# Performance work log

Measured on AMD Instinct MI355X. Metric: run time of the kernel, lower is better.

Reference implementation:

```python
import jax, jax.numpy as jnp
import numpy as np

NUM_EXPERTS = 8
TOP_K = 2
CAPACITY_FACTOR = 1.25
D_MODEL = 2048
HIDDEN = 2048
N_TOKENS = 4096


def _expert_capacity(n_tokens):
    ideal = TOP_K * n_tokens / NUM_EXPERTS
    allowed = int(CAPACITY_FACTOR * ideal)
    return ((allowed + 7) // 8) * 8  # ensure_multiple_of(..., 8)


def setup_inputs() -> dict:
    key = jax.random.key(0)
    ks = jax.random.split(key, 6)
    x = jax.random.normal(ks[0], (N_TOKENS, D_MODEL), dtype=jnp.float32)
    ew = jax.random.uniform(ks[1], (N_TOKENS, TOP_K), dtype=jnp.float32)
    expert_weights = ew / jnp.sum(ew, axis=-1, keepdims=True)  # router softmax-like weights
    expert_indices = jax.random.randint(ks[2], (N_TOKENS, TOP_K), 0, NUM_EXPERTS, dtype=jnp.int32)
    s = 1.0 / np.sqrt(D_MODEL)
    w1 = jax.random.normal(ks[3], (NUM_EXPERTS, D_MODEL, HIDDEN), dtype=jnp.float32) * s
    w3 = jax.random.normal(ks[4], (NUM_EXPERTS, D_MODEL, HIDDEN), dtype=jnp.float32) * s
    w2 = jax.random.normal(ks[5], (NUM_EXPERTS, HIDDEN, D_MODEL), dtype=jnp.float32) * (1.0 / np.sqrt(HIDDEN))
    return {"x": x, "expert_weights": expert_weights, "expert_indices": expert_indices,
            "w1": w1, "w2": w2, "w3": w3}


def reference(x, expert_weights, expert_indices, w1, w2, w3):
    N, d = x.shape
    E = NUM_EXPERTS
    cap = _expert_capacity(N)
    T = N * TOP_K

    flat_e = expert_indices.reshape(-1)                      # [T]
    # histc: tokens per expert
    counts = jnp.zeros((E,), jnp.int32).at[flat_e].add(1)
    # stable sort by expert id (torch.sort on ints is stable here semantically)
    order = jnp.argsort(flat_e, stable=True)                 # [T]
    sorted_e = flat_e[order]
    starts = jnp.cumsum(counts) - counts                     # bin start offsets
    pos = jnp.arange(T, dtype=jnp.int32) - starts[sorted_e]  # rank within expert bin
    valid = pos < cap                                        # drop tokens over capacity
    tok = order // TOP_K                                     # source token per routed slot

    # binned_gather -> [E, cap, d]
    dest = jnp.where(valid, sorted_e * cap + pos, 0)
    xg = jnp.zeros((E * cap, d), x.dtype).at[dest].add(
        jnp.where(valid[:, None], x[tok], 0.0))
    xg = xg.reshape(E, cap, d)

    # grouped SwiGLU MLP per expert
    h = jax.nn.silu(jnp.einsum('ecd,edh->ech', xg, w1)) * jnp.einsum('ecd,edh->ech', xg, w3)
    ye = jnp.einsum('ech,ehd->ecd', h, w2).reshape(E * cap, d)

    # binned_scatter with expert weights (combine)
    w_flat = expert_weights.reshape(-1)[order]               # [T]
    contrib = ye[dest] * (w_flat * valid.astype(x.dtype))[:, None]
    y = jnp.zeros((N, d), x.dtype).at[tok].add(contrib)
    return y, counts
```

## Files before the change

### kernel.cpp

```cpp
#include <hip/hip_runtime.h>
#include <cstdint>

#define NEXP 8
#define TOPK 2
#define NTOK 4096
#define NSLOT (NTOK * TOPK)
#define CAP 1280
#define DM 2048
#define EC (NEXP * CAP)

typedef __bf16 bf16x8 __attribute__((ext_vector_type(8)));
typedef float  f32x4  __attribute__((ext_vector_type(4)));
typedef int    i32x4  __attribute__((ext_vector_type(4)));
typedef int    i32x8  __attribute__((ext_vector_type(8)));

typedef const void __attribute__((address_space(1))) gvoid;
typedef void __attribute__((address_space(3))) lvoid;

__device__ __forceinline__ void gld16(const void* g, void* l) {
  __builtin_amdgcn_global_load_lds((gvoid*)(uintptr_t)g, (lvoid*)(uintptr_t)l,
                                   16, 0, 0);
}

__device__ __forceinline__ unsigned fp8x4(float a, float b, float c, float d) {
  int v = __builtin_amdgcn_cvt_pk_fp8_f32(a, b, 0, false);
  v = __builtin_amdgcn_cvt_pk_fp8_f32(c, d, v, true);
  return (unsigned)v;
}
__device__ __forceinline__ unsigned char fp8one(float a) {
  return (unsigned char)(__builtin_amdgcn_cvt_pk_fp8_f32(a, a, 0, false) & 0xff);
}

__global__ void route_k(const int* __restrict__ eidx, int* __restrict__ row_token,
                        int* __restrict__ slot_dest, int* __restrict__ mcount,
                        float* __restrict__ out) {
  __shared__ int lh[256][NEXP];
  int tid = threadIdx.x;
  for (int i = tid; i < EC; i += 256) row_token[i] = -1;
#pragma unroll
  for (int e = 0; e < NEXP; ++e) lh[tid][e] = 0;
  __syncthreads();
  int base = tid * 32;
  for (int j = 0; j < 32; ++j) lh[tid][eidx[base + j]]++;
  __syncthreads();
  if (tid < NEXP) {
    int run = 0;
    for (int i = 0; i < 256; ++i) { int t = lh[i][tid]; lh[i][tid] = run; run += t; }
    mcount[tid] = run < CAP ? run : CAP;
    out[(size_t)NTOK * DM + tid] = (float)run;
  }
  __syncthreads();
  for (int j = 0; j < 32; ++j) {
    int t = base + j;
    int e = eidx[t];
    int r = lh[tid][e]++;
    if (r < CAP) { int dst = e * CAP + r; slot_dest[t] = dst; row_token[dst] = t >> 1; }
    else slot_dest[t] = -1;
  }
}

__global__ void gather_k(const float* __restrict__ x, const int* __restrict__ row_token,
                         unsigned char* __restrict__ xg) {
  int r = blockIdx.x;
  int c = threadIdx.x * 8;
  int tok = row_token[r];
  uint2 o;
  if (tok >= 0) {
    const float* src = x + (size_t)tok * DM + c;
    float4 a = *(const float4*)src;
    float4 b = *(const float4*)(src + 4);
    o.x = fp8x4(a.x, a.y, a.z, a.w);
    o.y = fp8x4(b.x, b.y, b.z, b.w);
  } else {
    o.x = 0u; o.y = 0u;
  }
  *(uint2*)(xg + (size_t)r * DM + c) = o;
}

__global__ void transT_k(const float* __restrict__ w, unsigned char* __restrict__ wT) {
  __shared__ float t[64][69];
  int e = blockIdx.z;
  int n0 = blockIdx.x * 64, k0 = blockIdx.y * 64;
  const float* src = w + ((size_t)e << 22) + (size_t)k0 * DM + n0;
  unsigned char* dst = wT + ((size_t)e << 22) + (size_t)n0 * DM + k0;
  int c4 = (threadIdx.x & 15) * 4, r0 = threadIdx.x >> 4;
#pragma unroll
  for (int p = 0; p < 4; ++p) {
    int r = p * 16 + r0;
    float4 v = *(const float4*)(src + (size_t)r * DM + c4);
    t[r][c4 + 0] = v.x; t[r][c4 + 1] = v.y; t[r][c4 + 2] = v.z; t[r][c4 + 3] = v.w;
  }
  __syncthreads();
  int j = threadIdx.x & 7, rr0 = threadIdx.x >> 3;
#pragma unroll
  for (int q = 0; q < 2; ++q) {
    int rr = q * 32 + rr0;
    int k8 = j * 8;
    uint2 v;
    v.x = fp8x4(t[k8 + 0][rr], t[k8 + 1][rr], t[k8 + 2][rr], t[k8 + 3][rr]);
    v.y = fp8x4(t[k8 + 4][rr], t[k8 + 5][rr], t[k8 + 6][rr], t[k8 + 7][rr]);
    *(uint2*)(dst + (size_t)rr * DM + k8) = v;
  }
}

template<bool SWI>
__global__ __launch_bounds__(256, 4)
void gemm_k(const unsigned char* __restrict__ A0, const unsigned char* __restrict__ BT,
            void* C, const __bf16* __restrict__ U, const int* __restrict__ mcount) {
  int lbid = blockIdx.x + 16 * (blockIdx.y + 10 * blockIdx.z);
  int nb = (lbid & 7) * 160 + (lbid >> 3);
  int e = nb / 160, rem = nb % 160, mt = rem >> 4, nt = rem & 15;
  int mc = mcount[e];
  if (mt * 128 >= mc) return;

  __shared__ __align__(16) char smem[32 * 1024];
  char* lA = smem;
  char* lB = smem + 16384;

  int row0 = e * CAP + mt * 128;
  const unsigned char* gA = A0 + (size_t)row0 * DM;
  const unsigned char* gB = BT + ((size_t)e * DM + (size_t)nt * 128) * DM;

  int tid = threadIdx.x, w = tid >> 6, l = tid & 63;
  int wr = w >> 1, wc = w & 1;
  int lr = l & 15, kg = l >> 4;

  int sr = tid >> 3;
  int scs = (tid & 7) ^ (sr & 7);

  f32x4 acc[4][4];
#pragma unroll
  for (int m = 0; m < 4; ++m)
#pragma unroll
    for (int n = 0; n < 4; ++n)
#pragma unroll
      for (int j = 0; j < 4; ++j) acc[m][n][j] = 0.f;

  auto rdfrag = [&](const char* lX, int R) -> i32x8 {
    int r = R + lr;
    int a0 = r * 128 + (((2 * kg + 0) ^ (r & 7)) << 4);
    int a1 = r * 128 + (((2 * kg + 1) ^ (r & 7)) << 4);
    i32x4 lo = *(const i32x4*)(lX + a0);
    i32x4 hi = *(const i32x4*)(lX + a1);
    i32x8 v;
    v[0] = lo[0]; v[1] = lo[1]; v[2] = lo[2]; v[3] = lo[3];
    v[4] = hi[0]; v[5] = hi[1]; v[6] = hi[2]; v[7] = hi[3];
    return v;
  };

#pragma unroll 1
  for (int ks = 0; ks < 16; ++ks) {
#pragma unroll
    for (int s = 0; s < 4; ++s) {
      size_t goff = (size_t)(s * 32 + sr) * DM + (size_t)ks * 128 + scs * 16;
      gld16(gA + goff, lA + s * 4096 + w * 1024);
      gld16(gB + goff, lB + s * 4096 + w * 1024);
    }
    __syncthreads();
    i32x8 bf[4];
#pragma unroll
    for (int n = 0; n < 4; ++n) bf[n] = rdfrag(lB, wc * 64 + n * 16);
#pragma unroll
    for (int m = 0; m < 4; ++m) {
      i32x8 af = rdfrag(lA, wr * 64 + m * 16);
#pragma unroll
      for (int n = 0; n < 4; ++n)
        acc[m][n] = __builtin_amdgcn_mfma_scale_f32_16x16x128_f8f6f4(
            af, bf[n], acc[m][n], 0, 0, 0, 0x7F, 0, 0x7F);
    }
    __syncthreads();
  }

  int rg = l >> 4;
#pragma unroll
  for (int m = 0; m < 4; ++m)
#pragma unroll
    for (int n = 0; n < 4; ++n)
#pragma unroll
      for (int j = 0; j < 4; ++j) {
        int rr = row0 + wr * 64 + m * 16 + rg * 4 + j;
        int cc = nt * 128 + wc * 64 + n * 16 + lr;
        size_t off = (size_t)rr * DM + cc;
        float v = acc[m][n][j];
        if constexpr (SWI) {
          float u = (float)U[off];
          float s = u / (1.f + __expf(-u));
          ((unsigned char*)C)[off] = fp8one(s * v);
        } else {
          ((__bf16*)C)[off] = (__bf16)v;
        }
      }
}

__global__ void combine_k(const __bf16* __restrict__ ye, const int* __restrict__ slot_dest,
                          const float* __restrict__ ew, float* __restrict__ out) {
  int tok = blockIdx.x;
  int c = threadIdx.x * 8;
  int d0 = slot_dest[2 * tok], d1 = slot_dest[2 * tok + 1];
  float w0 = ew[2 * tok], w1 = ew[2 * tok + 1];
  float r[8];
#pragma unroll
  for (int j = 0; j < 8; ++j) r[j] = 0.f;
  if (d0 >= 0) {
    bf16x8 y0 = *(const bf16x8*)(ye + (size_t)d0 * DM + c);
#pragma unroll
    for (int j = 0; j < 8; ++j) r[j] += w0 * (float)y0[j];
  }
  if (d1 >= 0) {
    bf16x8 y1 = *(const bf16x8*)(ye + (size_t)d1 * DM + c);
#pragma unroll
    for (int j = 0; j < 8; ++j) r[j] += w1 * (float)y1[j];
  }
  float* dst = out + (size_t)tok * DM + c;
  float4 o0; o0.x = r[0]; o0.y = r[1]; o0.z = r[2]; o0.w = r[3];
  float4 o1; o1.x = r[4]; o1.y = r[5]; o1.z = r[6]; o1.w = r[7];
  *(float4*)dst = o0;
  *(float4*)(dst + 4) = o1;
}

extern "C" void kernel_launch(void* const* d_in, const int* in_sizes, int n_in,
                              void* d_out, int out_size, void* d_ws, size_t ws_size,
                              hipStream_t stream) {
  const float* x  = (const float*)d_in[0];
  const float* ew = (const float*)d_in[1];
  const int*   ei = (const int*)d_in[2];
  const float* w1 = (const float*)d_in[3];
  const float* w2 = (const float*)d_in[4];
  const float* w3 = (const float*)d_in[5];
  float* out = (float*)d_out;
  char* ws = (char*)d_ws;

  const size_t SZ8  = (size_t)EC * DM;
  const size_t SZ16 = 2 * SZ8;
  unsigned char* xg = (unsigned char*)ws;
  __bf16* uB = (__bf16*)(ws + SZ8);
  unsigned char* hB = (unsigned char*)(ws + SZ8 + SZ16);
  unsigned char* wT = (unsigned char*)(ws + 2 * SZ8 + SZ16);
  char* ints = ws + 2 * SZ8 + SZ16 + (size_t)NEXP * DM * DM;
  int* row_token = (int*)ints;
  int* slot_dest = row_token + EC;
  int* mcount    = slot_dest + NSLOT;

  dim3 tgrid(32, 32, NEXP);
  dim3 ggrid(16, 10, NEXP);

  route_k<<<1, 256, 0, stream>>>(ei, row_token, slot_dest, mcount, out);
  gather_k<<<EC, 256, 0, stream>>>(x, row_token, xg);

  transT_k<<<tgrid, 256, 0, stream>>>(w1, wT);
  gemm_k<false><<<ggrid, 256, 0, stream>>>(xg, wT, uB, nullptr, mcount);

  transT_k<<<tgrid, 256, 0, stream>>>(w3, wT);
  gemm_k<true><<<ggrid, 256, 0, stream>>>(xg, wT, hB, uB, mcount);

  transT_k<<<tgrid, 256, 0, stream>>>(w2, wT);
  gemm_k<false><<<ggrid, 256, 0, stream>>>(hB, wT, uB, nullptr, mcount);

  combine_k<<<NTOK, 256, 0, stream>>>(uB, slot_dest, ew, out);
}
```

Before: 315.8 us.

## Fuse gate and up projections into one dual-accumulator GEMM with SwiGLU epilogue

Replaces the separate w1 GEMM (writing bf16 intermediate) and w3 GEMM (reading it back for SwiGLU) with one kernel that loads each A tile once and multiplies it against both transposed w1 and w3 tiles, keeping two accumulator sets. SwiGLU is applied directly from registers and fp8 H is written. This removes the bf16 U round trip, one A reload and one kernel launch, at the cost of doubled accumulator registers, 48KB LDS, occupancy hint lowered to 2, and a second transposed-weight workspace buffer.

```diff
diff --git a/kernel.cpp b/kernel.cpp
--- a/kernel.cpp
+++ b/kernel.cpp
@@ -103,23 +103,26 @@
   }
 }
 
-template<bool SWI>
-__global__ __launch_bounds__(256, 4)
-void gemm_k(const unsigned char* __restrict__ A0, const unsigned char* __restrict__ BT,
-            void* C, const __bf16* __restrict__ U, const int* __restrict__ mcount) {
+__global__ __launch_bounds__(256, 2)
+void gemm13_k(const unsigned char* __restrict__ A0, const unsigned char* __restrict__ B1T,
+              const unsigned char* __restrict__ B3T, unsigned char* __restrict__ H,
+              const int* __restrict__ mcount) {
   int lbid = blockIdx.x + 16 * (blockIdx.y + 10 * blockIdx.z);
   int nb = (lbid & 7) * 160 + (lbid >> 3);
   int e = nb / 160, rem = nb % 160, mt = rem >> 4, nt = rem & 15;
   int mc = mcount[e];
   if (mt * 128 >= mc) return;
 
-  __shared__ __align__(16) char smem[32 * 1024];
-  char* lA = smem;
-  char* lB = smem + 16384;
+  __shared__ __align__(16) char smem[48 * 1024];
+  char* lA  = smem;
+  char* lB1 = smem + 16384;
+  char* lB3 = smem + 32768;
 
   int row0 = e * CAP + mt * 128;
-  const unsigned char* gA = A0 + (size_t)row0 * DM;
-  const unsigned char* gB = BT + ((size_t)e * DM + (size_t)nt * 128) * DM;
+  const unsigned char* gA  = A0 + (size_t)row0 * DM;
+  size_t boff = ((size_t)e * DM + (size_t)nt * 128) * DM;
+  const unsigned char* gB1 = B1T + boff;
+  const unsigned char* gB3 = B3T + boff;
 
   int tid = threadIdx.x, w = tid >> 6, l = tid & 63;
   int wr = w >> 1, wc = w & 1;
@@ -128,13 +131,13 @@
   int sr = tid >> 3;
   int scs = (tid & 7) ^ (sr & 7);
 
-  f32x4 acc[4][4];
+  f32x4 acc1[4][4], acc3[4][4];
 #pragma unroll
   for (int m = 0; m < 4; ++m)
 #pragma unroll
     for (int n = 0; n < 4; ++n)
 #pragma unroll
-      for (int j = 0; j < 4; ++j) acc[m][n][j] = 0.f;
+      for (int j = 0; j < 4; ++j) { acc1[m][n][j] = 0.f; acc3[m][n][j] = 0.f; }
 
   auto rdfrag = [&](const char* lX, int R) -> i32x8 {
     int r = R + lr;
@@ -153,6 +156,95 @@
 #pragma unroll
     for (int s = 0; s < 4; ++s) {
       size_t goff = (size_t)(s * 32 + sr) * DM + (size_t)ks * 128 + scs * 16;
+      gld16(gA  + goff, lA  + s * 4096 + w * 1024);
+      gld16(gB1 + goff, lB1 + s * 4096 + w * 1024);
+      gld16(gB3 + goff, lB3 + s * 4096 + w * 1024);
+    }
+    __syncthreads();
+    i32x8 bf1[4], bf3[4];
+#pragma unroll
+    for (int n = 0; n < 4; ++n) bf1[n] = rdfrag(lB1, wc * 64 + n * 16);
+#pragma unroll
+    for (int n = 0; n < 4; ++n) bf3[n] = rdfrag(lB3, wc * 64 + n * 16);
+#pragma unroll
+    for (int m = 0; m < 4; ++m) {
+      i32x8 af = rdfrag(lA, wr * 64 + m * 16);
+#pragma unroll
+      for (int n = 0; n < 4; ++n)
+        acc1[m][n] = __builtin_amdgcn_mfma_scale_f32_16x16x128_f8f6f4(
+            af, bf1[n], acc1[m][n], 0, 0, 0, 0x7F, 0, 0x7F);
+#pragma unroll
+      for (int n = 0; n < 4; ++n)
+        acc3[m][n] = __builtin_amdgcn_mfma_scale_f32_16x16x128_f8f6f4(
+            af, bf3[n], acc3[m][n], 0, 0, 0, 0x7F, 0, 0x7F);
+    }
+    __syncthreads();
+  }
+
+  int rg = l >> 4;
+#pragma unroll
+  for (int m = 0; m < 4; ++m)
+#pragma unroll
+    for (int n = 0; n < 4; ++n)
+#pragma unroll
+      for (int j = 0; j < 4; ++j) {
+        int rr = row0 + wr * 64 + m * 16 + rg * 4 + j;
+        int cc = nt * 128 + wc * 64 + n * 16 + lr;
+        float u = acc1[m][n][j];
+        float s = u / (1.f + __expf(-u));
+        H[(size_t)rr * DM + cc] = fp8one(s * acc3[m][n][j]);
+      }
+}
+
+__global__ __launch_bounds__(256, 4)
+void gemm_k(const unsigned char* __restrict__ A0, const unsigned char* __restrict__ BT,
+            __bf16* __restrict__ C, const int* __restrict__ mcount) {
+  int lbid = blockIdx.x + 16 * (blockIdx.y + 10 * blockIdx.z);
+  int nb = (lbid & 7) * 160 + (lbid >> 3);
+  int e = nb / 160, rem = nb % 160, mt = rem >> 4, nt = rem & 15;
+  int mc = mcount[e];
+  if (mt * 128 >= mc) return;
+
+  __shared__ __align__(16) char smem[32 * 1024];
+  char* lA = smem;
+  char* lB = smem + 16384;
+
+  int row0 = e * CAP + mt * 128;
+  const unsigned char* gA = A0 + (size_t)row0 * DM;
+  const unsigned char* gB = BT + ((size_t)e * DM + (size_t)nt * 128) * DM;
+
+  int tid = threadIdx.x, w = tid >> 6, l = tid & 63;
+  int wr = w >> 1, wc = w & 1;
+  int lr = l & 15, kg = l >> 4;
+
+  int sr = tid >> 3;
+  int scs = (tid & 7) ^ (sr & 7);
+
+  f32x4 acc[4][4];
+#pragma unroll
+  for (int m = 0; m < 4; ++m)
+#pragma unroll
+    for (int n = 0; n < 4; ++n)
+#pragma unroll
+      for (int j = 0; j < 4; ++j) acc[m][n][j] = 0.f;
+
+  auto rdfrag = [&](const char* lX, int R) -> i32x8 {
+    int r = R + lr;
+    int a0 = r * 128 + (((2 * kg + 0) ^ (r & 7)) << 4);
+    int a1 = r * 128 + (((2 * kg + 1) ^ (r & 7)) << 4);
+    i32x4 lo = *(const i32x4*)(lX + a0);
+    i32x4 hi = *(const i32x4*)(lX + a1);
+    i32x8 v;
+    v[0] = lo[0]; v[1] = lo[1]; v[2] = lo[2]; v[3] = lo[3];
+    v[4] = hi[0]; v[5] = hi[1]; v[6] = hi[2]; v[7] = hi[3];
+    return v;
+  };
+
+#pragma unroll 1
+  for (int ks = 0; ks < 16; ++ks) {
+#pragma unroll
+    for (int s = 0; s < 4; ++s) {
+      size_t goff = (size_t)(s * 32 + sr) * DM + (size_t)ks * 128 + scs * 16;
       gld16(gA + goff, lA + s * 4096 + w * 1024);
       gld16(gB + goff, lB + s * 4096 + w * 1024);
     }
@@ -180,15 +272,7 @@
       for (int j = 0; j < 4; ++j) {
         int rr = row0 + wr * 64 + m * 16 + rg * 4 + j;
         int cc = nt * 128 + wc * 64 + n * 16 + lr;
-        size_t off = (size_t)rr * DM + cc;
-        float v = acc[m][n][j];
-        if constexpr (SWI) {
-          float u = (float)U[off];
-          float s = u / (1.f + __expf(-u));
-          ((unsigned char*)C)[off] = fp8one(s * v);
-        } else {
-          ((__bf16*)C)[off] = (__bf16)v;
-        }
+        C[(size_t)rr * DM + cc] = (__bf16)acc[m][n][j];
       }
 }
 
@@ -232,11 +316,13 @@
 
   const size_t SZ8  = (size_t)EC * DM;
   const size_t SZ16 = 2 * SZ8;
-  unsigned char* xg = (unsigned char*)ws;
-  __bf16* uB = (__bf16*)(ws + SZ8);
-  unsigned char* hB = (unsigned char*)(ws + SZ8 + SZ16);
-  unsigned char* wT = (unsigned char*)(ws + 2 * SZ8 + SZ16);
-  char* ints = ws + 2 * SZ8 + SZ16 + (size_t)NEXP * DM * DM;
+  const size_t SZW  = (size_t)NEXP * DM * DM;
+  unsigned char* xg  = (unsigned char*)ws;
+  __bf16* yeB        = (__bf16*)(ws + SZ8);
+  unsigned char* hB  = (unsigned char*)(ws + SZ8 + SZ16);
+  unsigned char* wT1 = (unsigned char*)(ws + 2 * SZ8 + SZ16);
+  unsigned char* wT3 = (unsigned char*)(ws + 2 * SZ8 + SZ16 + SZW);
+  char* ints = ws + 2 * SZ8 + SZ16 + 2 * SZW;
   int* row_token = (int*)ints;
   int* slot_dest = row_token + EC;
   int* mcount    = slot_dest + NSLOT;
@@ -247,14 +333,12 @@
   route_k<<<1, 256, 0, stream>>>(ei, row_token, slot_dest, mcount, out);
   gather_k<<<EC, 256, 0, stream>>>(x, row_token, xg);
 
-  transT_k<<<tgrid, 256, 0, stream>>>(w1, wT);
-  gemm_k<false><<<ggrid, 256, 0, stream>>>(xg, wT, uB, nullptr, mcount);
-
-  transT_k<<<tgrid, 256, 0, stream>>>(w3, wT);
-  gemm_k<true><<<ggrid, 256, 0, stream>>>(xg, wT, hB, uB, mcount);
-
-  transT_k<<<tgrid, 256, 0, stream>>>(w2, wT);
-  gemm_k<false><<<ggrid, 256, 0, stream>>>(hB, wT, uB, nullptr, mcount);
-
-  combine_k<<<NTOK, 256, 0, stream>>>(uB, slot_dest, ew, out);
-}
+  transT_k<<<tgrid, 256, 0, stream>>>(w1, wT1);
+  transT_k<<<tgrid, 256, 0, stream>>>(w3, wT3);
+  gemm13_k<<<ggrid, 256, 0, stream>>>(xg, wT1, wT3, hB, mcount);
+
+  transT_k<<<tgrid, 256, 0, stream>>>(w2, wT1);
+  gemm_k<<<ggrid, 256, 0, stream>>>(hB, wT1, yeB, mcount);
+
+  combine_k<<<NTOK, 256, 0, stream>>>(yeB, slot_dest, ew, out);
+}
```

Result: faster. 303.6 us (-3.9%).
